# Optimization experiments

Measured on AMD Instinct MI355X. Metric: run time of the kernel, lower is better.

The kernel has to match this reference:

```python
import jax, jax.numpy as jnp
import numpy as np

N_NODES = 100000
N_EDGES = 1250000
IN_DIM, HID_DIM, OUT_DIM = 128, 64, 64
NUM_LAYERS = 3
EPS = 1e-12  # F.normalize eps


def setup_inputs() -> dict:
    key = jax.random.key(0)
    ks = jax.random.split(key, 10)
    s = 0.05
    x = jax.random.normal(ks[0], (N_NODES, IN_DIM), dtype=jnp.float32)
    edge_index = jax.random.randint(ks[1], (2, N_EDGES), 0, N_NODES, dtype=jnp.int32)
    W1 = jax.random.normal(ks[2], (IN_DIM, HID_DIM), dtype=jnp.float32) * s
    b1 = jax.random.normal(ks[3], (HID_DIM,), dtype=jnp.float32) * s
    Wl = jax.random.normal(ks[4], (NUM_LAYERS, HID_DIM, HID_DIM), dtype=jnp.float32) * s
    bl = jax.random.normal(ks[5], (NUM_LAYERS, HID_DIM), dtype=jnp.float32) * s
    Wr = jax.random.normal(ks[6], (NUM_LAYERS, HID_DIM, HID_DIM), dtype=jnp.float32) * s
    W2 = jax.random.normal(ks[7], (HID_DIM, OUT_DIM), dtype=jnp.float32) * s
    b2 = jax.random.normal(ks[8], (OUT_DIM,), dtype=jnp.float32) * s
    return {"x": x, "edge_index": edge_index, "W1": W1, "b1": b1,
            "Wl": Wl, "bl": bl, "Wr": Wr, "W2": W2, "b2": b2}


def reference(x, edge_index, W1, b1, Wl, bl, Wr, W2, b2):
    n = x.shape[0]
    src, dst = edge_index[0], edge_index[1]
    # in-degree for mean aggregation (zero-degree -> aggregate stays 0)
    deg = jax.ops.segment_sum(jnp.ones_like(dst, dtype=x.dtype), dst, num_segments=n)
    inv_deg = jnp.where(deg > 0, 1.0 / jnp.maximum(deg, 1.0), 0.0)[:, None]  # [n,1]
    h = x @ W1 + b1  # [n, hid]
    for i in range(Wl.shape[0]):
        # gather source features, scatter-mean to destinations
        agg = jax.ops.segment_sum(h[src], dst, num_segments=n) * inv_deg  # [n, hid]
        o = agg @ Wl[i] + bl[i] + h @ Wr[i]
        # row-wise L2 normalize (PyG normalize=True)
        norm = jnp.sqrt(jnp.sum(o * o, axis=-1, keepdims=True))
        o = o / jnp.maximum(norm, EPS)
        h = jax.nn.relu(o)
    return h @ W2 + b2
```

## Files before the change

### kernel.cpp

```cpp
#include <hip/hip_runtime.h>
#include <hip/hip_bf16.h>


#define NT 256
#define BATCH 4096
#define SBCAP 8192
#define HSTRIDE 72

typedef __attribute__((ext_vector_type(8))) short bf16x8;
typedef __attribute__((ext_vector_type(4))) float f32x4;

__device__ __forceinline__ float bfbits2f(unsigned short b) {
    return __uint_as_float(((unsigned)b) << 16);
}
__device__ __forceinline__ unsigned short f2bfbits(float v) {
    __hip_bfloat16 b = __float2bfloat16(v);
    return *reinterpret_cast<unsigned short*>(&b);
}


__global__ __launch_bounds__(NT) void bin1_kernel(const int* __restrict__ src,
    const int* __restrict__ dst, int m, unsigned* __restrict__ gcur,
    unsigned* __restrict__ bins) {
    __shared__ unsigned hist[256];
    __shared__ unsigned gbase[256];
    const int t = threadIdx.x;
    const int base = blockIdx.x * BATCH;
    hist[t] = 0;
    __syncthreads();
    int d[16], s[16];
    const int e0 = base + t * 16;
    const bool full = (base + BATCH) <= m;
    if (full) {
        #pragma unroll
        for (int q = 0; q < 4; ++q) {
            const int4 dv = *(const int4*)&dst[e0 + q * 4];
            const int4 sv = *(const int4*)&src[e0 + q * 4];
            d[q*4+0]=dv.x; d[q*4+1]=dv.y; d[q*4+2]=dv.z; d[q*4+3]=dv.w;
            s[q*4+0]=sv.x; s[q*4+1]=sv.y; s[q*4+2]=sv.z; s[q*4+3]=sv.w;
        }
        #pragma unroll
        for (int q = 0; q < 16; ++q) atomicAdd(&hist[d[q] >> 9], 1u);
    } else {
        #pragma unroll
        for (int q = 0; q < 16; ++q) {
            const int e = e0 + q;
            if (e < m) { d[q] = dst[e]; s[q] = src[e]; atomicAdd(&hist[d[q] >> 9], 1u); }
            else d[q] = -1;
        }
    }
    __syncthreads();
    {
        const unsigned h = hist[t];
        gbase[t] = h ? atomicAdd(&gcur[t], h) : 0u;
        hist[t] = 0;
    }
    __syncthreads();
    if (full) {
        #pragma unroll
        for (int q = 0; q < 16; ++q) {
            const int b = d[q] >> 9;
            const unsigned slot = gbase[b] + atomicAdd(&hist[b], 1u);
            bins[(size_t)b * SBCAP + slot] = ((unsigned)s[q] << 9) | (unsigned)(d[q] & 511);
        }
    } else {
        #pragma unroll
        for (int q = 0; q < 16; ++q) {
            if (d[q] >= 0) {
                const int b = d[q] >> 9;
                const unsigned slot = gbase[b] + atomicAdd(&hist[b], 1u);
                bins[(size_t)b * SBCAP + slot] = ((unsigned)s[q] << 9) | (unsigned)(d[q] & 511);
            }
        }
    }
}

__global__ __launch_bounds__(NT) void bin2_kernel(const unsigned* __restrict__ bins,
    const unsigned* __restrict__ gcur, int* __restrict__ row_ptr, int* __restrict__ csr,
    int n, int nsb, int m) {
    __shared__ unsigned hist[512];
    __shared__ unsigned off[512];
    __shared__ unsigned cur[512];
    __shared__ unsigned wsum[4];
    __shared__ unsigned gpre[256];
    const int k = blockIdx.x;
    const int t = threadIdx.x;
    const int lane = t & 63, wid = t >> 6;

    {
        const unsigned gv = (t < nsb) ? gcur[t] : 0u;
        unsigned gx = gv;
        #pragma unroll
        for (int o = 1; o < 64; o <<= 1) {
            const unsigned tt = __shfl_up(gx, o, 64);
            if (lane >= o) gx += tt;
        }
        if (lane == 63) wsum[wid] = gx;
        __syncthreads();
        unsigned wo = 0;
        for (int w = 0; w < wid; ++w) wo += wsum[w];
        gpre[t] = wo + gx - gv;
        __syncthreads();
    }
    const int cnt = (int)gcur[k];
    const unsigned sb = gpre[k];
    if (k == 0 && t == 0) row_ptr[n] = m;

    const unsigned* reg = bins + (size_t)k * SBCAP;
    hist[2*t] = 0; hist[2*t+1] = 0;
    __syncthreads();
    for (int i = t; i < cnt; i += NT) atomicAdd(&hist[reg[i] & 511u], 1u);
    __syncthreads();
    const unsigned v0 = hist[2*t], v1 = hist[2*t+1];
    const unsigned ps = v0 + v1;
    unsigned x = ps;
    #pragma unroll
    for (int o = 1; o < 64; o <<= 1) {
        const unsigned tt = __shfl_up(x, o, 64);
        if (lane >= o) x += tt;
    }
    if (lane == 63) wsum[wid] = x;
    __syncthreads();
    unsigned woff = 0;
    for (int w = 0; w < wid; ++w) woff += wsum[w];
    const unsigned excl = woff + x - ps;
    off[2*t] = excl; off[2*t+1] = excl + v0;
    cur[2*t] = 0; cur[2*t+1] = 0;
    const int node = k * 512 + 2 * t;
    if (node < n)     row_ptr[node]     = (int)(sb + excl);
    if (node + 1 < n) row_ptr[node + 1] = (int)(sb + excl + v0);
    __syncthreads();
    for (int i = t; i < cnt; i += NT) {
        const unsigned u = reg[i];
        const unsigned l = u & 511u;
        const unsigned r = atomicAdd(&cur[l], 1u);
        csr[sb + off[l] + r] = (int)(u >> 9);
    }
}


__global__ void wconv_kernel(const float* __restrict__ W1, const float* __restrict__ Wl,
                             const float* __restrict__ Wr, const float* __restrict__ W2,
                             unsigned short* __restrict__ out, unsigned* __restrict__ gcur,
                             int nsb) {
    int i = blockIdx.x * blockDim.x + threadIdx.x;
    if (i < nsb) gcur[i] = 0u;
    if (i >= 36864) return;
    float v;
    if (i < 8192) {
        const int col = i >> 7, k = i & 127;
        v = W1[k * 64 + col];
    } else if (i < 32768) {
        const int j = i - 8192;
        const int mm = j >> 13, r = j & 8191;
        const int isR = (r >> 12) & 1, q = r & 4095;
        const int col = q >> 6, k = q & 63;
        v = (isR ? Wr : Wl)[mm * 4096 + k * 64 + col];
    } else {
        const int q = i - 32768;
        const int col = q >> 6, k = q & 63;
        v = W2[k * 64 + col];
    }
    out[i] = f2bfbits(v);
}


__global__ __launch_bounds__(NT) void agg_kernel(const unsigned short* __restrict__ h,
    const int* __restrict__ row_ptr, const int* __restrict__ csr,
    unsigned short* __restrict__ aggB, int n) {
    const int t = threadIdx.x;
    const int lane = t & 63;
    const int half = lane >> 5;
    const int gs = (lane >> 4) & 1;
    const int c = lane & 15;
    const int gw = (blockIdx.x * NT + t) >> 6;
    const int nw = (gridDim.x * NT) >> 6;
    const int npairs = (n + 1) >> 1;
    for (int p = gw; p < npairs; p += nw) {
        const int node = p * 2 + half;
        const bool valid = node < n;
        const int node_c = valid ? node : (n - 1);
        const int rs = row_ptr[node_c];
        const int re = row_ptr[node_c + 1];
        float a0 = 0.f, a1 = 0.f, a2 = 0.f, a3 = 0.f;
        {
            int ce[8], si[8];
            #pragma unroll
            for (int i = 0; i < 8; ++i) {
                const int e = rs + 2 * i + gs;
                ce[i] = (e < re) ? e : 0;
            }
            #pragma unroll
            for (int i = 0; i < 8; ++i) si[i] = csr[ce[i]];
            ushort4 v[8];
            #pragma unroll
            for (int i = 0; i < 8; ++i) v[i] = *(const ushort4*)&h[(size_t)si[i] * 64 + c * 4];
            #pragma unroll
            for (int i = 0; i < 8; ++i) {
                if (rs + 2 * i + gs < re) {
                    a0 += bfbits2f(v[i].x);
                    a1 += bfbits2f(v[i].y);
                    a2 += bfbits2f(v[i].z);
                    a3 += bfbits2f(v[i].w);
                }
            }
        }
        for (int base = rs + 16; base < re; base += 8) {
            int ce[4], si[4];
            #pragma unroll
            for (int i = 0; i < 4; ++i) {
                const int e = base + 2 * i + gs;
                ce[i] = (e < re) ? e : 0;
            }
            #pragma unroll
            for (int i = 0; i < 4; ++i) si[i] = csr[ce[i]];
            ushort4 v[4];
            #pragma unroll
            for (int i = 0; i < 4; ++i) v[i] = *(const ushort4*)&h[(size_t)si[i] * 64 + c * 4];
            #pragma unroll
            for (int i = 0; i < 4; ++i) {
                if (base + 2 * i + gs < re) {
                    a0 += bfbits2f(v[i].x);
                    a1 += bfbits2f(v[i].y);
                    a2 += bfbits2f(v[i].z);
                    a3 += bfbits2f(v[i].w);
                }
            }
        }
        a0 += __shfl_xor(a0, 16, 64);
        a1 += __shfl_xor(a1, 16, 64);
        a2 += __shfl_xor(a2, 16, 64);
        a3 += __shfl_xor(a3, 16, 64);
        if (gs == 0 && valid) {
            const float inv = (re > rs) ? (1.0f / (float)(re - rs)) : 0.0f;
            ushort4 o;
            o.x = f2bfbits(a0 * inv);
            o.y = f2bfbits(a1 * inv);
            o.z = f2bfbits(a2 * inv);
            o.w = f2bfbits(a3 * inv);
            *(ushort4*)&aggB[(size_t)node * 64 + c * 4] = o;
        }
    }
}


template<int A1F32, int LAST>
__global__ __launch_bounds__(NT) void gemm_mfma(
    const float* __restrict__ A1f, const unsigned short* __restrict__ A1b,
    int ldA1, int K1, const unsigned short* __restrict__ W1t,
    const unsigned short* __restrict__ A2b, const unsigned short* __restrict__ W2t,
    const float* __restrict__ bias, float* __restrict__ outF,
    unsigned short* __restrict__ outB, int n, int do_norm,
    const unsigned short* __restrict__ W2t2, const float* __restrict__ b2) {
    const int t = threadIdx.x;
    const int lane = t & 63;
    const int w = t >> 6;
    const int r16 = lane & 15;
    const int g = lane >> 4;
    const int row0 = blockIdx.x * 128 + w * 32;

    f32x4 acc[2][4];
    #pragma unroll
    for (int i = 0; i < 2; ++i)
        #pragma unroll
        for (int j = 0; j < 4; ++j) {
            acc[i][j][0] = 0.f; acc[i][j][1] = 0.f; acc[i][j][2] = 0.f; acc[i][j][3] = 0.f;
        }

    int ra[2];
    #pragma unroll
    for (int rt = 0; rt < 2; ++rt) {
        int r = row0 + rt * 16 + r16;
        ra[rt] = (r < n) ? r : (n - 1);
    }

    #pragma unroll 1
    for (int kc = 0; kc < K1; kc += 32) {
        bf16x8 af[2];
        #pragma unroll
        for (int rt = 0; rt < 2; ++rt) {
            if (A1F32) {
                const float* p = &A1f[(size_t)ra[rt] * ldA1 + kc + g * 8];
                const float4 f0 = *(const float4*)p;
                const float4 f1 = *(const float4*)(p + 4);
                bf16x8 a;
                a[0] = (short)f2bfbits(f0.x); a[1] = (short)f2bfbits(f0.y);
                a[2] = (short)f2bfbits(f0.z); a[3] = (short)f2bfbits(f0.w);
                a[4] = (short)f2bfbits(f1.x); a[5] = (short)f2bfbits(f1.y);
                a[6] = (short)f2bfbits(f1.z); a[7] = (short)f2bfbits(f1.w);
                af[rt] = a;
            } else {
                af[rt] = *(const bf16x8*)&A1b[(size_t)ra[rt] * ldA1 + kc + g * 8];
            }
        }
        #pragma unroll
        for (int ct = 0; ct < 4; ++ct) {
            const bf16x8 bw = *(const bf16x8*)&W1t[(size_t)(ct * 16 + r16) * K1 + kc + g * 8];
            acc[0][ct] = __builtin_amdgcn_mfma_f32_16x16x32_bf16(af[0], bw, acc[0][ct], 0, 0, 0);
            acc[1][ct] = __builtin_amdgcn_mfma_f32_16x16x32_bf16(af[1], bw, acc[1][ct], 0, 0, 0);
        }
    }
    if (A2b) {
        #pragma unroll 1
        for (int kc = 0; kc < 64; kc += 32) {
            bf16x8 af[2];
            #pragma unroll
            for (int rt = 0; rt < 2; ++rt)
                af[rt] = *(const bf16x8*)&A2b[(size_t)ra[rt] * 64 + kc + g * 8];
            #pragma unroll
            for (int ct = 0; ct < 4; ++ct) {
                const bf16x8 bw = *(const bf16x8*)&W2t[(size_t)(ct * 16 + r16) * 64 + kc + g * 8];
                acc[0][ct] = __builtin_amdgcn_mfma_f32_16x16x32_bf16(af[0], bw, acc[0][ct], 0, 0, 0);
                acc[1][ct] = __builtin_amdgcn_mfma_f32_16x16x32_bf16(af[1], bw, acc[1][ct], 0, 0, 0);
            }
        }
    }

    float bcol[4];
    #pragma unroll
    for (int ct = 0; ct < 4; ++ct) bcol[ct] = bias[ct * 16 + r16];

    #pragma unroll
    for (int rt = 0; rt < 2; ++rt) {
        #pragma unroll
        for (int ct = 0; ct < 4; ++ct)
            #pragma unroll
            for (int reg = 0; reg < 4; ++reg) acc[rt][ct][reg] += bcol[ct];

        if (do_norm) {
            #pragma unroll
            for (int reg = 0; reg < 4; ++reg) {
                float ss = 0.f;
                #pragma unroll
                for (int ct = 0; ct < 4; ++ct) ss += acc[rt][ct][reg] * acc[rt][ct][reg];
                ss += __shfl_xor(ss, 1, 64);
                ss += __shfl_xor(ss, 2, 64);
                ss += __shfl_xor(ss, 4, 64);
                ss += __shfl_xor(ss, 8, 64);
                const float inv = 1.0f / fmaxf(sqrtf(ss), 1e-12f);
                #pragma unroll
                for (int ct = 0; ct < 4; ++ct)
                    acc[rt][ct][reg] = fmaxf(acc[rt][ct][reg] * inv, 0.0f);
            }
        }
    }

    if constexpr (!LAST) {
        #pragma unroll
        for (int rt = 0; rt < 2; ++rt) {
            const int rbase = row0 + rt * 16 + g * 4;
            #pragma unroll
            for (int reg = 0; reg < 4; ++reg) {
                const int rr = rbase + reg;
                if (rr < n) {
                    if (outB) {
                        #pragma unroll
                        for (int ct = 0; ct < 4; ++ct)
                            outB[(size_t)rr * 64 + ct * 16 + r16] = f2bfbits(acc[rt][ct][reg]);
                    } else {
                        #pragma unroll
                        for (int ct = 0; ct < 4; ++ct)
                            outF[(size_t)rr * 64 + ct * 16 + r16] = acc[rt][ct][reg];
                    }
                }
            }
        }
    } else {
        __shared__ unsigned short h3S[128][HSTRIDE];
        #pragma unroll
        for (int rt = 0; rt < 2; ++rt) {
            #pragma unroll
            for (int reg = 0; reg < 4; ++reg) {
                const int lr = w * 32 + rt * 16 + g * 4 + reg;
                #pragma unroll
                for (int ct = 0; ct < 4; ++ct)
                    h3S[lr][ct * 16 + r16] = f2bfbits(acc[rt][ct][reg]);
            }
        }
        __syncthreads();
        f32x4 acc2[2][4];
        #pragma unroll
        for (int i = 0; i < 2; ++i)
            #pragma unroll
            for (int j = 0; j < 4; ++j) { acc2[i][j][0]=0.f; acc2[i][j][1]=0.f; acc2[i][j][2]=0.f; acc2[i][j][3]=0.f; }
        #pragma unroll
        for (int kc = 0; kc < 64; kc += 32) {
            bf16x8 af[2];
            #pragma unroll
            for (int rt = 0; rt < 2; ++rt)
                af[rt] = *(const bf16x8*)&h3S[w * 32 + rt * 16 + r16][kc + g * 8];
            #pragma unroll
            for (int ct = 0; ct < 4; ++ct) {
                const bf16x8 bw = *(const bf16x8*)&W2t2[(size_t)(ct * 16 + r16) * 64 + kc + g * 8];
                acc2[0][ct] = __builtin_amdgcn_mfma_f32_16x16x32_bf16(af[0], bw, acc2[0][ct], 0, 0, 0);
                acc2[1][ct] = __builtin_amdgcn_mfma_f32_16x16x32_bf16(af[1], bw, acc2[1][ct], 0, 0, 0);
            }
        }
        float b2c[4];
        #pragma unroll
        for (int ct = 0; ct < 4; ++ct) b2c[ct] = b2[ct * 16 + r16];
        #pragma unroll
        for (int rt = 0; rt < 2; ++rt) {
            const int rbase = row0 + rt * 16 + g * 4;
            #pragma unroll
            for (int reg = 0; reg < 4; ++reg) {
                const int rr = rbase + reg;
                if (rr < n) {
                    #pragma unroll
                    for (int ct = 0; ct < 4; ++ct)
                        outF[(size_t)rr * 64 + ct * 16 + r16] = acc2[rt][ct][reg] + b2c[ct];
                }
            }
        }
    }
}


extern "C" void kernel_launch(void* const* d_in, const int* in_sizes, int n_in,
                              void* d_out, int out_size, void* d_ws, size_t ws_size,
                              hipStream_t stream) {
    const float* x  = (const float*)d_in[0];
    const int*   ei = (const int*)  d_in[1];
    const float* W1 = (const float*)d_in[2];
    const float* b1 = (const float*)d_in[3];
    const float* Wl = (const float*)d_in[4];
    const float* bl = (const float*)d_in[5];
    const float* Wr = (const float*)d_in[6];
    const float* W2 = (const float*)d_in[7];
    const float* b2 = (const float*)d_in[8];
    float* out = (float*)d_out;

    const int n = in_sizes[0] / 128;
    const int m = in_sizes[1] / 2;
    const int* src = ei;
    const int* dst = ei + m;

    const int nsb = (n + 511) >> 9;

    char* ws = (char*)d_ws;
    size_t off = 0;
    auto alloc = [&](size_t bytes) -> void* {
        void* p = ws + off;
        off = (off + bytes + 255) & ~(size_t)255;
        return p;
    };
    unsigned short* aggB    = (unsigned short*)alloc((size_t)n * 64 * 2);
    unsigned short* hbf     = (unsigned short*)alloc((size_t)n * 64 * 2);
    int*            row_ptr = (int*)alloc((size_t)(n + 1) * sizeof(int));
    unsigned*       gcur    = (unsigned*)alloc((size_t)nsb * 4);
    unsigned*       bins    = (unsigned*)alloc((size_t)nsb * SBCAP * 4);
    int*            csr     = (int*)alloc((size_t)m * 4);
    unsigned short* wt      = (unsigned short*)alloc(36864 * 2);

    const unsigned short* W1t = wt;
    const unsigned short* W2t = wt + 32768;

    const int nb1 = (m + BATCH - 1) / BATCH;
    const int gtiles = (n + 127) / 128;

    wconv_kernel<<<144, NT, 0, stream>>>(W1, Wl, Wr, W2, wt, gcur, nsb);

    gemm_mfma<1, 0><<<gtiles, NT, 0, stream>>>(x, nullptr, 128, 128, W1t,
                                               nullptr, nullptr, b1, nullptr, hbf, n, 0,
                                               nullptr, nullptr);

    bin1_kernel<<<nb1, NT, 0, stream>>>(src, dst, m, gcur, bins);
    bin2_kernel<<<nsb, NT, 0, stream>>>(bins, gcur, row_ptr, csr, n, nsb, m);

    for (int i = 0; i < 2; ++i) {
        agg_kernel<<<2048, NT, 0, stream>>>(hbf, row_ptr, csr, aggB, n);
        const unsigned short* Wlt = wt + 8192 + (size_t)i * 8192;
        const unsigned short* Wrt = Wlt + 4096;
        gemm_mfma<0, 0><<<gtiles, NT, 0, stream>>>(nullptr, aggB, 64, 64, Wlt,
                                                   hbf, Wrt, bl + (size_t)i * 64,
                                                   nullptr, hbf, n, 1, nullptr, nullptr);
    }
    agg_kernel<<<2048, NT, 0, stream>>>(hbf, row_ptr, csr, aggB, n);
    gemm_mfma<0, 1><<<gtiles, NT, 0, stream>>>(nullptr, aggB, 64, 64, wt + 8192 + 16384,
                                               hbf, wt + 8192 + 16384 + 4096, bl + 128,
                                               out, nullptr, n, 1, W2t, b2);
}
```

Measured before the change: 198.0 us.

## Merge independent setup kernels via block-range dispatch and specialize the layer GEMM

The weight conversion is folded into the first edge-binning kernel, and the input linear layer is folded into the CSR-building kernel. Both merges use disjoint block ranges, so independent work shares a launch and can run concurrently. Zeroing the bin counters moves to a memset. The layer GEMM drops its runtime branches and fuses the two K loops into one unrolled loop that interleaves the aggregate and self MFMAs. This removes launches and tail idle time, at the cost of higher register and LDS use in the combined kernels.

```diff
diff --git a/kernel.cpp b/kernel.cpp
--- a/kernel.cpp
+++ b/kernel.cpp
@@ -6,6 +6,7 @@
 #define BATCH 4096
 #define SBCAP 8192
 #define HSTRIDE 72
+#define WCONV_BLOCKS 144
 
 typedef __attribute__((ext_vector_type(8))) short bf16x8;
 typedef __attribute__((ext_vector_type(4))) float f32x4;
@@ -19,13 +20,38 @@
 }
 
 
-__global__ __launch_bounds__(NT) void bin1_kernel(const int* __restrict__ src,
-    const int* __restrict__ dst, int m, unsigned* __restrict__ gcur,
-    unsigned* __restrict__ bins) {
+__global__ __launch_bounds__(NT) void wconv_bin1_kernel(
+    const float* __restrict__ W1, const float* __restrict__ Wl,
+    const float* __restrict__ Wr, const float* __restrict__ W2,
+    unsigned short* __restrict__ wt,
+    const int* __restrict__ src, const int* __restrict__ dst, int m,
+    unsigned* __restrict__ gcur, unsigned* __restrict__ bins) {
+    const int t = threadIdx.x;
+    if ((int)blockIdx.x < WCONV_BLOCKS) {
+        const int i = blockIdx.x * NT + t;
+        if (i >= 36864) return;
+        float v;
+        if (i < 8192) {
+            const int col = i >> 7, k = i & 127;
+            v = W1[k * 64 + col];
+        } else if (i < 32768) {
+            const int j = i - 8192;
+            const int mm = j >> 13, r = j & 8191;
+            const int isR = (r >> 12) & 1, q = r & 4095;
+            const int col = q >> 6, k = q & 63;
+            v = (isR ? Wr : Wl)[mm * 4096 + k * 64 + col];
+        } else {
+            const int q = i - 32768;
+            const int col = q >> 6, k = q & 63;
+            v = W2[k * 64 + col];
+        }
+        wt[i] = f2bfbits(v);
+        return;
+    }
     __shared__ unsigned hist[256];
     __shared__ unsigned gbase[256];
-    const int t = threadIdx.x;
-    const int base = blockIdx.x * BATCH;
+    const int bb = (int)blockIdx.x - WCONV_BLOCKS;
+    const int base = bb * BATCH;
     hist[t] = 0;
     __syncthreads();
     int d[16], s[16];
@@ -75,16 +101,87 @@
     }
 }
 
-__global__ __launch_bounds__(NT) void bin2_kernel(const unsigned* __restrict__ bins,
-    const unsigned* __restrict__ gcur, int* __restrict__ row_ptr, int* __restrict__ csr,
-    int n, int nsb, int m) {
+
+__device__ __forceinline__ void lin1_body(const float* __restrict__ x,
+    const unsigned short* __restrict__ W1t, const float* __restrict__ b1,
+    unsigned short* __restrict__ hbf, int n, int bid) {
+    const int t = threadIdx.x;
+    const int lane = t & 63;
+    const int w = t >> 6;
+    const int r16 = lane & 15;
+    const int g = lane >> 4;
+    const int row0 = bid * 128 + w * 32;
+
+    f32x4 acc[2][4];
+    #pragma unroll
+    for (int i = 0; i < 2; ++i)
+        #pragma unroll
+        for (int j = 0; j < 4; ++j) { acc[i][j][0]=0.f; acc[i][j][1]=0.f; acc[i][j][2]=0.f; acc[i][j][3]=0.f; }
+
+    int ra[2];
+    #pragma unroll
+    for (int rt = 0; rt < 2; ++rt) {
+        const int r = row0 + rt * 16 + r16;
+        ra[rt] = (r < n) ? r : (n - 1);
+    }
+
+    #pragma unroll 1
+    for (int kc = 0; kc < 128; kc += 32) {
+        bf16x8 af[2];
+        #pragma unroll
+        for (int rt = 0; rt < 2; ++rt) {
+            const float* p = &x[(size_t)ra[rt] * 128 + kc + g * 8];
+            const float4 f0 = *(const float4*)p;
+            const float4 f1 = *(const float4*)(p + 4);
+            bf16x8 a;
+            a[0] = (short)f2bfbits(f0.x); a[1] = (short)f2bfbits(f0.y);
+            a[2] = (short)f2bfbits(f0.z); a[3] = (short)f2bfbits(f0.w);
+            a[4] = (short)f2bfbits(f1.x); a[5] = (short)f2bfbits(f1.y);
+            a[6] = (short)f2bfbits(f1.z); a[7] = (short)f2bfbits(f1.w);
+            af[rt] = a;
+        }
+        #pragma unroll
+        for (int ct = 0; ct < 4; ++ct) {
+            const bf16x8 bw = *(const bf16x8*)&W1t[(size_t)(ct * 16 + r16) * 128 + kc + g * 8];
+            acc[0][ct] = __builtin_amdgcn_mfma_f32_16x16x32_bf16(af[0], bw, acc[0][ct], 0, 0, 0);
+            acc[1][ct] = __builtin_amdgcn_mfma_f32_16x16x32_bf16(af[1], bw, acc[1][ct], 0, 0, 0);
+        }
+    }
+
+    float bcol[4];
+    #pragma unroll
+    for (int ct = 0; ct < 4; ++ct) bcol[ct] = b1[ct * 16 + r16];
+    #pragma unroll
+    for (int rt = 0; rt < 2; ++rt) {
+        const int rbase = row0 + rt * 16 + g * 4;
+        #pragma unroll
+        for (int reg = 0; reg < 4; ++reg) {
+            const int rr = rbase + reg;
+            if (rr < n) {
+                #pragma unroll
+                for (int ct = 0; ct < 4; ++ct)
+                    hbf[(size_t)rr * 64 + ct * 16 + r16] = f2bfbits(acc[rt][ct][reg] + bcol[ct]);
+            }
+        }
+    }
+}
+
+__global__ __launch_bounds__(NT) void bin2_lin1_kernel(
+    const unsigned* __restrict__ bins, const unsigned* __restrict__ gcur,
+    int* __restrict__ row_ptr, int* __restrict__ csr, int n, int nsb, int m,
+    const float* __restrict__ x, const unsigned short* __restrict__ W1t,
+    const float* __restrict__ b1, unsigned short* __restrict__ hbf) {
     __shared__ unsigned hist[512];
     __shared__ unsigned off[512];
     __shared__ unsigned cur[512];
     __shared__ unsigned wsum[4];
     __shared__ unsigned gpre[256];
+    const int t = threadIdx.x;
+    if ((int)blockIdx.x >= nsb) {
+        lin1_body(x, W1t, b1, hbf, n, (int)blockIdx.x - nsb);
+        return;
+    }
     const int k = blockIdx.x;
-    const int t = threadIdx.x;
     const int lane = t & 63, wid = t >> 6;
 
     {
@@ -113,17 +210,17 @@
     __syncthreads();
     const unsigned v0 = hist[2*t], v1 = hist[2*t+1];
     const unsigned ps = v0 + v1;
-    unsigned x = ps;
+    unsigned x2 = ps;
     #pragma unroll
     for (int o = 1; o < 64; o <<= 1) {
-        const unsigned tt = __shfl_up(x, o, 64);
-        if (lane >= o) x += tt;
-    }
-    if (lane == 63) wsum[wid] = x;
+        const unsigned tt = __shfl_up(x2, o, 64);
+        if (lane >= o) x2 += tt;
+    }
+    if (lane == 63) wsum[wid] = x2;
     __syncthreads();
     unsigned woff = 0;
     for (int w = 0; w < wid; ++w) woff += wsum[w];
-    const unsigned excl = woff + x - ps;
+    const unsigned excl = woff + x2 - ps;
     off[2*t] = excl; off[2*t+1] = excl + v0;
     cur[2*t] = 0; cur[2*t+1] = 0;
     const int node = k * 512 + 2 * t;
@@ -136,32 +233,6 @@
         const unsigned r = atomicAdd(&cur[l], 1u);
         csr[sb + off[l] + r] = (int)(u >> 9);
     }
-}
-
-
-__global__ void wconv_kernel(const float* __restrict__ W1, const float* __restrict__ Wl,
-                             const float* __restrict__ Wr, const float* __restrict__ W2,
-                             unsigned short* __restrict__ out, unsigned* __restrict__ gcur,
-                             int nsb) {
-    int i = blockIdx.x * blockDim.x + threadIdx.x;
-    if (i < nsb) gcur[i] = 0u;
-    if (i >= 36864) return;
-    float v;
-    if (i < 8192) {
-        const int col = i >> 7, k = i & 127;
-        v = W1[k * 64 + col];
-    } else if (i < 32768) {
-        const int j = i - 8192;
-        const int mm = j >> 13, r = j & 8191;
-        const int isR = (r >> 12) & 1, q = r & 4095;
-        const int col = q >> 6, k = q & 63;
-        v = (isR ? Wr : Wl)[mm * 4096 + k * 64 + col];
-    } else {
-        const int q = i - 32768;
-        const int col = q >> 6, k = q & 63;
-        v = W2[k * 64 + col];
-    }
-    out[i] = f2bfbits(v);
 }
 
 
@@ -244,13 +315,12 @@
 }
 
 
-template<int A1F32, int LAST>
+template<int LAST>
 __global__ __launch_bounds__(NT) void gemm_mfma(
-    const float* __restrict__ A1f, const unsigned short* __restrict__ A1b,
-    int ldA1, int K1, const unsigned short* __restrict__ W1t,
+    const unsigned short* __restrict__ A1b, const unsigned short* __restrict__ W1t,
     const unsigned short* __restrict__ A2b, const unsigned short* __restrict__ W2t,
     const float* __restrict__ bias, float* __restrict__ outF,
-    unsigned short* __restrict__ outB, int n, int do_norm,
+    unsigned short* __restrict__ outB, int n,
     const unsigned short* __restrict__ W2t2, const float* __restrict__ b2) {
     const int t = threadIdx.x;
     const int lane = t & 63;
@@ -274,45 +344,22 @@
         ra[rt] = (r < n) ? r : (n - 1);
     }
 
-    #pragma unroll 1
-    for (int kc = 0; kc < K1; kc += 32) {
-        bf16x8 af[2];
+    #pragma unroll
+    for (int kc = 0; kc < 64; kc += 32) {
+        bf16x8 a1[2], a2[2];
         #pragma unroll
         for (int rt = 0; rt < 2; ++rt) {
-            if (A1F32) {
-                const float* p = &A1f[(size_t)ra[rt] * ldA1 + kc + g * 8];
-                const float4 f0 = *(const float4*)p;
-                const float4 f1 = *(const float4*)(p + 4);
-                bf16x8 a;
-                a[0] = (short)f2bfbits(f0.x); a[1] = (short)f2bfbits(f0.y);
-                a[2] = (short)f2bfbits(f0.z); a[3] = (short)f2bfbits(f0.w);
-                a[4] = (short)f2bfbits(f1.x); a[5] = (short)f2bfbits(f1.y);
-                a[6] = (short)f2bfbits(f1.z); a[7] = (short)f2bfbits(f1.w);
-                af[rt] = a;
-            } else {
-                af[rt] = *(const bf16x8*)&A1b[(size_t)ra[rt] * ldA1 + kc + g * 8];
-            }
+            a1[rt] = *(const bf16x8*)&A1b[(size_t)ra[rt] * 64 + kc + g * 8];
+            a2[rt] = *(const bf16x8*)&A2b[(size_t)ra[rt] * 64 + kc + g * 8];
         }
         #pragma unroll
         for (int ct = 0; ct < 4; ++ct) {
-            const bf16x8 bw = *(const bf16x8*)&W1t[(size_t)(ct * 16 + r16) * K1 + kc + g * 8];
-            acc[0][ct] = __builtin_amdgcn_mfma_f32_16x16x32_bf16(af[0], bw, acc[0][ct], 0, 0, 0);
-            acc[1][ct] = __builtin_amdgcn_mfma_f32_16x16x32_bf16(af[1], bw, acc[1][ct], 0, 0, 0);
-        }
-    }
-    if (A2b) {
-        #pragma unroll 1
-        for (int kc = 0; kc < 64; kc += 32) {
-            bf16x8 af[2];
-            #pragma unroll
-            for (int rt = 0; rt < 2; ++rt)
-                af[rt] = *(const bf16x8*)&A2b[(size_t)ra[rt] * 64 + kc + g * 8];
-            #pragma unroll
-            for (int ct = 0; ct < 4; ++ct) {
-                const bf16x8 bw = *(const bf16x8*)&W2t[(size_t)(ct * 16 + r16) * 64 + kc + g * 8];
-                acc[0][ct] = __builtin_amdgcn_mfma_f32_16x16x32_bf16(af[0], bw, acc[0][ct], 0, 0, 0);
-                acc[1][ct] = __builtin_amdgcn_mfma_f32_16x16x32_bf16(af[1], bw, acc[1][ct], 0, 0, 0);
-            }
+            const bf16x8 bw1 = *(const bf16x8*)&W1t[(size_t)(ct * 16 + r16) * 64 + kc + g * 8];
+            const bf16x8 bw2 = *(const bf16x8*)&W2t[(size_t)(ct * 16 + r16) * 64 + kc + g * 8];
+            acc[0][ct] = __builtin_amdgcn_mfma_f32_16x16x32_bf16(a1[0], bw1, acc[0][ct], 0, 0, 0);
+            acc[0][ct] = __builtin_amdgcn_mfma_f32_16x16x32_bf16(a2[0], bw2, acc[0][ct], 0, 0, 0);
+            acc[1][ct] = __builtin_amdgcn_mfma_f32_16x16x32_bf16(a1[1], bw1, acc[1][ct], 0, 0, 0);
+            acc[1][ct] = __builtin_amdgcn_mfma_f32_16x16x32_bf16(a2[1], bw2, acc[1][ct], 0, 0, 0);
         }
     }
 
@@ -327,21 +374,19 @@
             #pragma unroll
             for (int reg = 0; reg < 4; ++reg) acc[rt][ct][reg] += bcol[ct];
 
-        if (do_norm) {
-            #pragma unroll
-            for (int reg = 0; reg < 4; ++reg) {
-                float ss = 0.f;
-                #pragma unroll
-                for (int ct = 0; ct < 4; ++ct) ss += acc[rt][ct][reg] * acc[rt][ct][reg];
-                ss += __shfl_xor(ss, 1, 64);
-                ss += __shfl_xor(ss, 2, 64);
-                ss += __shfl_xor(ss, 4, 64);
-                ss += __shfl_xor(ss, 8, 64);
-                const float inv = 1.0f / fmaxf(sqrtf(ss), 1e-12f);
-                #pragma unroll
-                for (int ct = 0; ct < 4; ++ct)
-                    acc[rt][ct][reg] = fmaxf(acc[rt][ct][reg] * inv, 0.0f);
-            }
+        #pragma unroll
+        for (int reg = 0; reg < 4; ++reg) {
+            float ss = 0.f;
+            #pragma unroll
+            for (int ct = 0; ct < 4; ++ct) ss += acc[rt][ct][reg] * acc[rt][ct][reg];
+            ss += __shfl_xor(ss, 1, 64);
+            ss += __shfl_xor(ss, 2, 64);
+            ss += __shfl_xor(ss, 4, 64);
+            ss += __shfl_xor(ss, 8, 64);
+            const float inv = 1.0f / fmaxf(sqrtf(ss), 1e-12f);
+            #pragma unroll
+            for (int ct = 0; ct < 4; ++ct)
+                acc[rt][ct][reg] = fmaxf(acc[rt][ct][reg] * inv, 0.0f);
         }
     }
 
@@ -353,15 +398,9 @@
             for (int reg = 0; reg < 4; ++reg) {
                 const int rr = rbase + reg;
                 if (rr < n) {
-                    if (outB) {
-                        #pragma unroll
-                        for (int ct = 0; ct < 4; ++ct)
-                            outB[(size_t)rr * 64 + ct * 16 + r16] = f2bfbits(acc[rt][ct][reg]);
-                    } else {
-                        #pragma unroll
-                        for (int ct = 0; ct < 4; ++ct)
-                            outF[(size_t)rr * 64 + ct * 16 + r16] = acc[rt][ct][reg];
-                    }
+                    #pragma unroll
+                    for (int ct = 0; ct < 4; ++ct)
+                        outB[(size_t)rr * 64 + ct * 16 + r16] = f2bfbits(acc[rt][ct][reg]);
                 }
             }
         }
@@ -458,25 +497,23 @@
     const int nb1 = (m + BATCH - 1) / BATCH;
     const int gtiles = (n + 127) / 128;
 
-    wconv_kernel<<<144, NT, 0, stream>>>(W1, Wl, Wr, W2, wt, gcur, nsb);
-
-    gemm_mfma<1, 0><<<gtiles, NT, 0, stream>>>(x, nullptr, 128, 128, W1t,
-                                               nullptr, nullptr, b1, nullptr, hbf, n, 0,
-                                               nullptr, nullptr);
-
-    bin1_kernel<<<nb1, NT, 0, stream>>>(src, dst, m, gcur, bins);
-    bin2_kernel<<<nsb, NT, 0, stream>>>(bins, gcur, row_ptr, csr, n, nsb, m);
+    hipMemsetAsync(gcur, 0, (size_t)nsb * 4, stream);
+
+    wconv_bin1_kernel<<<WCONV_BLOCKS + nb1, NT, 0, stream>>>(W1, Wl, Wr, W2, wt,
+                                                             src, dst, m, gcur, bins);
+    bin2_lin1_kernel<<<nsb + gtiles, NT, 0, stream>>>(bins, gcur, row_ptr, csr, n, nsb, m,
+                                                      x, W1t, b1, hbf);
 
     for (int i = 0; i < 2; ++i) {
         agg_kernel<<<2048, NT, 0, stream>>>(hbf, row_ptr, csr, aggB, n);
         const unsigned short* Wlt = wt + 8192 + (size_t)i * 8192;
         const unsigned short* Wrt = Wlt + 4096;
-        gemm_mfma<0, 0><<<gtiles, NT, 0, stream>>>(nullptr, aggB, 64, 64, Wlt,
-                                                   hbf, Wrt, bl + (size_t)i * 64,
-                                                   nullptr, hbf, n, 1, nullptr, nullptr);
+        gemm_mfma<0><<<gtiles, NT, 0, stream>>>(aggB, Wlt, hbf, Wrt,
+                                                bl + (size_t)i * 64,
+                                                nullptr, hbf, n, nullptr, nullptr);
     }
     agg_kernel<<<2048, NT, 0, stream>>>(hbf, row_ptr, csr, aggB, n);
-    gemm_mfma<0, 1><<<gtiles, NT, 0, stream>>>(nullptr, aggB, 64, 64, wt + 8192 + 16384,
-                                               hbf, wt + 8192 + 16384 + 4096, bl + 128,
-                                               out, nullptr, n, 1, W2t, b2);
-}
+    gemm_mfma<1><<<gtiles, NT, 0, stream>>>(aggB, wt + 8192 + 16384,
+                                            hbf, wt + 8192 + 16384 + 4096,
+                                            bl + 128, out, nullptr, n, W2t, b2);
+}
```

Result: faster. 188.4 us (-4.8%).
